# Kernel optimization log

Measured on AMD Instinct MI355X. Metric: run time of the kernel, lower is better.

Reference implementation:

```python
import jax, jax.numpy as jnp
import numpy as np

D_MODEL = 1024
N_HEADS = 16
D_K = D_MODEL // N_HEADS
ROPE_THETA = 10000.0


def setup_inputs() -> dict:
    key = jax.random.key(0)
    ks = jax.random.split(key, 5)
    B, S = 2, 2048
    std = (2.0 / (D_MODEL + D_MODEL)) ** 0.5
    x = jax.random.normal(ks[0], (B, S, D_MODEL), dtype=jnp.float32)
    Wq = jax.random.normal(ks[1], (D_MODEL, D_MODEL), dtype=jnp.float32) * std
    Wk = jax.random.normal(ks[2], (D_MODEL, D_MODEL), dtype=jnp.float32) * std
    Wv = jax.random.normal(ks[3], (D_MODEL, D_MODEL), dtype=jnp.float32) * std
    Wo = jax.random.normal(ks[4], (D_MODEL, D_MODEL), dtype=jnp.float32) * std
    token_positions = jnp.arange(S, dtype=jnp.int64 if jax.config.jax_enable_x64 else jnp.int32)
    return {"x": x, "Wq": Wq, "Wk": Wk, "Wv": Wv, "Wo": Wo,
            "token_positions": token_positions}


def _apply_rope(t, token_positions):
    # t: [B, H, S, d_k]; token_positions: [S]
    inv_freq = 1.0 / (ROPE_THETA ** (jnp.arange(0, D_K, 2, dtype=jnp.float32) / D_K))  # [d_k/2]
    freqs = token_positions.astype(jnp.float32)[:, None] * inv_freq[None, :]  # [S, d_k/2]
    cos, sin = jnp.cos(freqs), jnp.sin(freqs)
    x1, x2 = t[..., ::2], t[..., 1::2]
    xr = x1 * cos - x2 * sin
    yr = x1 * sin + x2 * cos
    # interleave back to even/odd positions
    out = jnp.stack([xr, yr], axis=-1).reshape(t.shape)
    return out


def reference(x, Wq, Wk, Wv, Wo, token_positions):
    B, S, D = x.shape
    H, dk = N_HEADS, D_K
    # projections: weight is [d_out, d_in], applied as x @ W.T
    def proj_heads(W):
        y = jnp.einsum('bsd,ed->bse', x, W)
        return y.reshape(B, S, H, dk).transpose(0, 2, 1, 3)  # [B,H,S,dk]
    q = proj_heads(Wq)
    k = proj_heads(Wk)
    v = proj_heads(Wv)
    q = _apply_rope(q, token_positions)
    k = _apply_rope(k, token_positions)
    scores = jnp.einsum('bhqd,bhkd->bhqk', q, k) / jnp.sqrt(jnp.float32(dk))
    causal = jnp.tril(jnp.ones((S, S), dtype=bool))
    scores = jnp.where(causal, scores, -jnp.inf)
    attn = jax.nn.softmax(scores, axis=-1)
    out = jnp.einsum('bhqk,bhkd->bhqd', attn, v)  # [B,H,S,dk]
    out = out.transpose(0, 2, 1, 3).reshape(B, S, D)
    return jnp.einsum('bsd,ed->bse', out, Wo)
```

## Files before the change

### kernel.cpp

```cpp
#include <hip/hip_runtime.h>

typedef __bf16 bf16x8 __attribute__((ext_vector_type(8)));
typedef float f32x4 __attribute__((ext_vector_type(4)));
typedef unsigned short u16x8 __attribute__((ext_vector_type(8)));


__device__ __forceinline__ unsigned short f2bf(float f) {
  unsigned u = __builtin_bit_cast(unsigned, f);
  u = (u + 0x7FFFu + ((u >> 16) & 1u)) >> 16;
  return (unsigned short)u;
}

__device__ __forceinline__ float bf2f(unsigned short v) {
  return __builtin_bit_cast(float, ((unsigned)v) << 16);
}

__device__ __forceinline__ unsigned cvt_pk_bf16(float lo, float hi) {
  unsigned r;
  asm("v_cvt_pk_bf16_f32 %0, %1, %2" : "=v"(r) : "v"(lo), "v"(hi));
  return r;
}

__device__ __forceinline__ void load_lds16(const void* g, void* l) {
  __builtin_amdgcn_global_load_lds(
      (__attribute__((address_space(1))) void*)g,
      (__attribute__((address_space(3))) void*)l, 16, 0, 0);
}

__global__ __launch_bounds__(256) void k_convert(
    const float* __restrict__ x,
    const float* __restrict__ wq, const float* __restrict__ wk,
    const float* __restrict__ wv, const float* __restrict__ wo,
    unsigned short* __restrict__ xb,
    unsigned short* __restrict__ wqb, unsigned short* __restrict__ wkb,
    unsigned short* __restrict__ wvb, unsigned short* __restrict__ wob) {
  const int g = blockIdx.x * 256 + threadIdx.x;
  const float* src;
  unsigned short* dst;
  int off;
  if (g < (1 << 20)) {
    src = x; dst = xb; off = g;
  } else {
    const int q = g - (1 << 20);
    const int t = q >> 18;
    off = q & ((1 << 18) - 1);
    src = (t == 0) ? wq : (t == 1) ? wk : (t == 2) ? wv : wo;
    dst = (t == 0) ? wqb : (t == 1) ? wkb : (t == 2) ? wvb : wob;
  }
  const float4 v = ((const float4*)src)[off];
  ushort4 r;
  r.x = f2bf(v.x); r.y = f2bf(v.y); r.z = f2bf(v.z); r.w = f2bf(v.w);
  ((ushort4*)dst)[off] = r;
}

__global__ __launch_bounds__(256) void k_rope_tab(const int* __restrict__ tpos,
                                                  float* __restrict__ ct,
                                                  float* __restrict__ st) {
  const int idx = blockIdx.x * 256 + threadIdx.x;
  const int s = idx >> 5, i = idx & 31;
  const double p = (double)tpos[s];
  const double f = p * pow(10000.0, -(double)(2 * i) / 64.0);
  ct[idx] = (float)cos(f);
  st[idx] = (float)sin(f);
}

__device__ __forceinline__ void gemm_core_1024(
    const unsigned short* __restrict__ Ag,
    const unsigned short* __restrict__ Bg,
    unsigned short* As, unsigned short* Bs, f32x4 (&acc)[4][4], int tid) {
  const int lane = tid & 63;
  const int w = tid >> 6;
  const int wm = (w >> 1) * 64;
  const int wn = (w & 1) * 64;
  const int lr = lane & 15;
  const int lg8 = (lane >> 4) * 8;
  const int c0 = tid, c1 = 256 + tid;
  const int ar0 = c0 >> 2, ac0 = (c0 & 3) * 8;
  const int ar1 = c1 >> 2, ac1 = (c1 & 3) * 8;

  auto stage = [&](int buf, int kt) {
    unsigned short* Ab = As + buf * 4096;
    unsigned short* Bb = Bs + buf * 4096;
    load_lds16(Ag + ar0 * 1024 + kt + ac0, Ab + c0 * 8);
    load_lds16(Ag + ar1 * 1024 + kt + ac1, Ab + c1 * 8);
    load_lds16(Bg + ar0 * 1024 + kt + ac0, Bb + c0 * 8);
    load_lds16(Bg + ar1 * 1024 + kt + ac1, Bb + c1 * 8);
  };

  stage(0, 0);
  stage(1, 32);
  int cur = 0;
  for (int ki = 0; ki < 32; ++ki) {
    if (ki + 2 < 32) {
      int nb = cur + 2; if (nb >= 3) nb -= 3;
      stage(nb, (ki + 2) * 32);
      asm volatile("s_waitcnt vmcnt(8)" ::: "memory");
    } else if (ki + 1 < 32) {
      asm volatile("s_waitcnt vmcnt(4)" ::: "memory");
    } else {
      asm volatile("s_waitcnt vmcnt(0)" ::: "memory");
    }
    __builtin_amdgcn_s_barrier();
    const unsigned short* Ab = As + cur * 4096;
    const unsigned short* Bb = Bs + cur * 4096;
    bf16x8 af[4], bfv[4];
#pragma unroll
    for (int mi = 0; mi < 4; ++mi)
      af[mi] = *(const bf16x8*)(Ab + (wm + mi * 16 + lr) * 32 + lg8);
#pragma unroll
    for (int ni = 0; ni < 4; ++ni)
      bfv[ni] = *(const bf16x8*)(Bb + (wn + ni * 16 + lr) * 32 + lg8);
    __builtin_amdgcn_s_setprio(1);
#pragma unroll
    for (int mi = 0; mi < 4; ++mi)
#pragma unroll
      for (int ni = 0; ni < 4; ++ni)
        acc[mi][ni] = __builtin_amdgcn_mfma_f32_16x16x32_bf16(
            af[mi], bfv[ni], acc[mi][ni], 0, 0, 0);
    __builtin_amdgcn_s_setprio(0);
    __builtin_amdgcn_s_barrier();
    ++cur; if (cur == 3) cur = 0;
  }
}

__device__ __forceinline__ void gemm_core_bm64(
    const unsigned short* __restrict__ Ag,
    const unsigned short* __restrict__ Bg,
    unsigned short* As, unsigned short* Bs, f32x4 (&acc)[2][4], int tid) {
  const int lane = tid & 63;
  const int w = tid >> 6;
  const int wm = (w >> 1) * 32;
  const int wn = (w & 1) * 64;
  const int lr = lane & 15;
  const int lg8 = (lane >> 4) * 8;
  const int ar = tid >> 2, ac = (tid & 3) * 8;
  const int c0 = tid, c1 = 256 + tid;
  const int br0 = c0 >> 2, bc0 = (c0 & 3) * 8;
  const int br1 = c1 >> 2, bc1 = (c1 & 3) * 8;

  auto stage = [&](int buf, int kt) {
    load_lds16(Ag + ar * 1024 + kt + ac, As + buf * 2048 + tid * 8);
    load_lds16(Bg + br0 * 1024 + kt + bc0, Bs + buf * 4096 + c0 * 8);
    load_lds16(Bg + br1 * 1024 + kt + bc1, Bs + buf * 4096 + c1 * 8);
  };

  stage(0, 0);
  stage(1, 32);
  int cur = 0;
  for (int ki = 0; ki < 32; ++ki) {
    if (ki + 2 < 32) {
      int nb = cur + 2; if (nb >= 3) nb -= 3;
      stage(nb, (ki + 2) * 32);
      asm volatile("s_waitcnt vmcnt(6)" ::: "memory");
    } else if (ki + 1 < 32) {
      asm volatile("s_waitcnt vmcnt(3)" ::: "memory");
    } else {
      asm volatile("s_waitcnt vmcnt(0)" ::: "memory");
    }
    __builtin_amdgcn_s_barrier();
    const unsigned short* Ab = As + cur * 2048;
    const unsigned short* Bb = Bs + cur * 4096;
    bf16x8 af[2], bfv[4];
#pragma unroll
    for (int mi = 0; mi < 2; ++mi)
      af[mi] = *(const bf16x8*)(Ab + (wm + mi * 16 + lr) * 32 + lg8);
#pragma unroll
    for (int ni = 0; ni < 4; ++ni)
      bfv[ni] = *(const bf16x8*)(Bb + (wn + ni * 16 + lr) * 32 + lg8);
    __builtin_amdgcn_s_setprio(1);
#pragma unroll
    for (int mi = 0; mi < 2; ++mi)
#pragma unroll
      for (int ni = 0; ni < 4; ++ni)
        acc[mi][ni] = __builtin_amdgcn_mfma_f32_16x16x32_bf16(
            af[mi], bfv[ni], acc[mi][ni], 0, 0, 0);
    __builtin_amdgcn_s_setprio(0);
    __builtin_amdgcn_s_barrier();
    ++cur; if (cur == 3) cur = 0;
  }
}

__global__ __launch_bounds__(256) void k_proj(
    const unsigned short* __restrict__ Xb,
    const unsigned short* __restrict__ Wq, const unsigned short* __restrict__ Wk,
    const unsigned short* __restrict__ Wv,
    const float* __restrict__ ctab, const float* __restrict__ stab,
    unsigned short* __restrict__ Qo, unsigned short* __restrict__ Ko,
    unsigned short* __restrict__ Vo) {
  __shared__ __align__(16) unsigned short As[3 * 128 * 32];
  __shared__ __align__(16) unsigned short Bs[3 * 128 * 32];
  const int z = blockIdx.z;
  const unsigned short* Wsel = (z == 0) ? Wq : (z == 1) ? Wk : Wv;
  unsigned short* Out = (z == 0) ? Qo : (z == 1) ? Ko : Vo;
  const int tid = threadIdx.x;
  const int bm = blockIdx.x * 128, bn = blockIdx.y * 128;
  f32x4 acc[4][4] = {};
  gemm_core_1024(Xb + (size_t)bm * 1024, Wsel + (size_t)bn * 1024, As, Bs, acc, tid);

  const int lane = tid & 63, w = tid >> 6;
  const int wm = (w >> 1) * 64, wn = (w & 1) * 64;
  const int lr = lane & 15, lg = lane >> 4;

  if (z == 2) {
#pragma unroll
    for (int mi = 0; mi < 4; ++mi) {
      const int r0 = bm + wm + mi * 16 + lg * 4;
      const int s = r0 & 2047, b = r0 >> 11;
#pragma unroll
      for (int ni = 0; ni < 4; ++ni) {
        const int e = bn + wn + ni * 16 + lr;
        const int h = e >> 6, d = e & 63;
        ushort4 pk;
        pk.x = f2bf(acc[mi][ni][0]);
        pk.y = f2bf(acc[mi][ni][1]);
        pk.z = f2bf(acc[mi][ni][2]);
        pk.w = f2bf(acc[mi][ni][3]);
        *(ushort4*)&Out[((size_t)(b * 16 + h) * 64 + d) * 2048 + s] = pk;
      }
    }
    return;
  }

  const bool odd = lane & 1;
#pragma unroll
  for (int mi = 0; mi < 4; ++mi) {
#pragma unroll
    for (int ni = 0; ni < 4; ++ni) {
#pragma unroll
      for (int reg = 0; reg < 4; ++reg) {
        const int r = bm + wm + mi * 16 + lg * 4 + reg;
        const int e = bn + wn + ni * 16 + lr;
        float val = acc[mi][ni][reg];
        const float partner = __shfl_xor(val, 1);
        const int s = r & 2047, b = r >> 11;
        const int h = e >> 6, d = e & 63;
        const int i = d >> 1;
        const float c = ctab[s * 32 + i];
        const float sn = stab[s * 32 + i];
        const float outv = odd ? (val * c + partner * sn) : (val * c - partner * sn);
        Out[((size_t)(b * 16 + h) * 2048 + s) * 64 + d] = f2bf(outv);
      }
    }
  }
}

__global__ __launch_bounds__(64, 4) void k_attn(
    const unsigned short* __restrict__ Q, const unsigned short* __restrict__ K,
    const unsigned short* __restrict__ Vt, unsigned short* __restrict__ O,
    unsigned short* __restrict__ OpLo, unsigned short* __restrict__ OpHi,
    float2* __restrict__ mlLo, float2* __restrict__ mlHi) {
  __shared__ __align__(16) unsigned short Vs[64 * 64];
  __shared__ __align__(16) unsigned short Pl[16 * 64];
  const int L = blockIdx.x;
  const int i = L >> 3;
  const int bh = (L & 7) * 4 + (i & 3);
  const int c = i >> 2;
  int s, k0, k1, mode;
  if (c < 60) {
    s = 127 - c; const int T = (s * 16 + 79) >> 6; k0 = T >> 1; k1 = T; mode = 2;
  } else if (c < 120) {
    s = 127 - (c - 60); const int T = (s * 16 + 79) >> 6; k0 = 0; k1 = T >> 1; mode = 1;
  } else {
    s = 187 - c; k0 = 0; k1 = (s * 16 + 79) >> 6; mode = 0;
  }
  const int qrow = s * 16;
  const bool masklast = (mode != 1);
  const int lane = threadIdx.x & 63;
  const int lr = lane & 15, lg = lane >> 4;
  const unsigned short* Qg = Q + (size_t)bh * 2048 * 64;
  const unsigned short* Kg = K + (size_t)bh * 2048 * 64;
  const unsigned short* Vg = Vt + (size_t)bh * 64 * 2048;

  bf16x8 qf[2];
#pragma unroll
  for (int h = 0; h < 2; ++h)
    qf[h] = *(const bf16x8*)(Qg + (qrow + lr) * 64 + h * 32 + lg * 8);

  u16x8 ouv;
#pragma unroll
  for (int j = 0; j < 8; ++j) ouv[j] = 0x3F80;
  const bf16x8 onesf = __builtin_bit_cast(bf16x8, ouv);

  f32x4 oacc[4] = {};
  f32x4 la = {};
  float m = -__builtin_inff();

  const float SCL = 0.125f * 1.44269504088896f;

  const int kbase = lr * 64 + lg * 8;
  const int vbase = (lane >> 3) * 2048 + (((lane & 7) ^ (lane >> 3)) * 8);
  const int psw = (lr & 7) << 3;

  auto issueV = [&](int kv) {
    const unsigned short* src = Vg + kv * 64 + vbase;
    unsigned short* dst = &Vs[0] + lane * 8;
#pragma unroll
    for (int i0 = 0; i0 < 8; ++i0)
      load_lds16(src + i0 * 16384, dst + i0 * 512);
  };

  issueV(k0);
  for (int t = k0; t < k1; ++t) {
    bf16x8 kb[4][2];
    {
      const unsigned short* base = Kg + (size_t)t * 4096 + kbase;
#pragma unroll
      for (int nt = 0; nt < 4; ++nt)
#pragma unroll
        for (int h = 0; h < 2; ++h)
          kb[nt][h] = *(const bf16x8*)(base + nt * 1024 + h * 32);
    }

    f32x4 sacc[4];
    __builtin_amdgcn_s_setprio(1);
#pragma unroll
    for (int nt = 0; nt < 4; ++nt) {
      f32x4 z = {0.f, 0.f, 0.f, 0.f};
      z = __builtin_amdgcn_mfma_f32_16x16x32_bf16(kb[nt][0], qf[0], z, 0, 0, 0);
      sacc[nt] = __builtin_amdgcn_mfma_f32_16x16x32_bf16(kb[nt][1], qf[1], z, 0, 0, 0);
    }
    __builtin_amdgcn_s_setprio(0);

    if (masklast && t == k1 - 1) {
      const int qg = qrow + lr;
#pragma unroll
      for (int nt = 0; nt < 4; ++nt)
#pragma unroll
        for (int reg = 0; reg < 4; ++reg) {
          const int kg = t * 64 + nt * 16 + lg * 4 + reg;
          if (kg > qg) sacc[nt][reg] = -__builtin_inff();
        }
    }

    float t0 = fmaxf(fmaxf(sacc[0][0], sacc[0][1]), fmaxf(sacc[0][2], sacc[0][3]));
    float t1 = fmaxf(fmaxf(sacc[1][0], sacc[1][1]), fmaxf(sacc[1][2], sacc[1][3]));
    float t2 = fmaxf(fmaxf(sacc[2][0], sacc[2][1]), fmaxf(sacc[2][2], sacc[2][3]));
    float t3 = fmaxf(fmaxf(sacc[3][0], sacc[3][1]), fmaxf(sacc[3][2], sacc[3][3]));
    float pm = fmaxf(fmaxf(t0, t1), fmaxf(t2, t3));
    pm = fmaxf(pm, __shfl_xor(pm, 16));
    pm = fmaxf(pm, __shfl_xor(pm, 32));
    if (__any(pm > m)) {
      const float mn = fmaxf(m, pm);
      const float al = exp2f(SCL * (m - mn));
      m = mn;
#pragma unroll
      for (int reg = 0; reg < 4; ++reg) la[reg] *= al;
#pragma unroll
      for (int nt = 0; nt < 4; ++nt)
#pragma unroll
        for (int reg = 0; reg < 4; ++reg) oacc[nt][reg] *= al;
    }
    const float msc = SCL * m;

#pragma unroll
    for (int nt = 0; nt < 4; ++nt) {
      const float p0 = exp2f(sacc[nt][0] * SCL - msc);
      const float p1 = exp2f(sacc[nt][1] * SCL - msc);
      const float p2 = exp2f(sacc[nt][2] * SCL - msc);
      const float p3 = exp2f(sacc[nt][3] * SCL - msc);
      const unsigned w01 = cvt_pk_bf16(p0, p1);
      const unsigned w23 = cvt_pk_bf16(p2, p3);
      ushort4 pk;
      pk.x = (unsigned short)w01; pk.y = (unsigned short)(w01 >> 16);
      pk.z = (unsigned short)w23; pk.w = (unsigned short)(w23 >> 16);
      *(ushort4*)(Pl + lr * 64 + ((nt * 16 + lg * 4) ^ psw)) = pk;
    }
    bf16x8 pa[2];
#pragma unroll
    for (int ks = 0; ks < 2; ++ks)
      pa[ks] = *(const bf16x8*)(Pl + lr * 64 + ((ks * 32 + lg * 8) ^ psw));

    asm volatile("s_waitcnt vmcnt(0)" ::: "memory");

    __builtin_amdgcn_s_setprio(1);
    la = __builtin_amdgcn_mfma_f32_16x16x32_bf16(onesf, pa[0], la, 0, 0, 0);
    la = __builtin_amdgcn_mfma_f32_16x16x32_bf16(onesf, pa[1], la, 0, 0, 0);
#pragma unroll
    for (int nt = 0; nt < 4; ++nt) {
      const int row = nt * 16 + lr;
      const bf16x8 vb0 = *(const bf16x8*)(Vs + row * 64 + ((lg ^ (row & 7)) * 8));
      const bf16x8 vb1 = *(const bf16x8*)(Vs + row * 64 + (((lg + 4) ^ (row & 7)) * 8));
      oacc[nt] = __builtin_amdgcn_mfma_f32_16x16x32_bf16(vb0, pa[0], oacc[nt], 0, 0, 0);
      oacc[nt] = __builtin_amdgcn_mfma_f32_16x16x32_bf16(vb1, pa[1], oacc[nt], 0, 0, 0);
    }
    __builtin_amdgcn_s_setprio(0);

    asm volatile("s_waitcnt lgkmcnt(0)" ::: "memory");
    if (t + 1 < k1) issueV(t + 1);
  }

  const int b = bh >> 4, h = bh & 15;
  if (mode == 0) {
    const float inv = 1.0f / la[0];
    unsigned short* dst = &O[((size_t)b * 2048 + qrow + lr) * 1024 + h * 64];
#pragma unroll
    for (int nt = 0; nt < 4; ++nt) {
      const unsigned w01 = cvt_pk_bf16(oacc[nt][0] * inv, oacc[nt][1] * inv);
      const unsigned w23 = cvt_pk_bf16(oacc[nt][2] * inv, oacc[nt][3] * inv);
      ushort4 pk;
      pk.x = (unsigned short)w01; pk.y = (unsigned short)(w01 >> 16);
      pk.z = (unsigned short)w23; pk.w = (unsigned short)(w23 >> 16);
      *(ushort4*)(dst + nt * 16 + lg * 4) = pk;
    }
  } else {
    const int idx = bh * 60 + (s - 68);
    unsigned short* dst = (mode == 1 ? OpLo : OpHi) + idx * 1024 + lr * 64;
#pragma unroll
    for (int nt = 0; nt < 4; ++nt) {
      const unsigned w01 = cvt_pk_bf16(oacc[nt][0], oacc[nt][1]);
      const unsigned w23 = cvt_pk_bf16(oacc[nt][2], oacc[nt][3]);
      ushort4 pk;
      pk.x = (unsigned short)w01; pk.y = (unsigned short)(w01 >> 16);
      pk.z = (unsigned short)w23; pk.w = (unsigned short)(w23 >> 16);
      *(ushort4*)(dst + nt * 16 + lg * 4) = pk;
    }
    if (lane < 16)
      (mode == 1 ? mlLo : mlHi)[idx * 16 + lr] = make_float2(m, la[0]);
  }
}

__global__ __launch_bounds__(256) void k_merge(
    const unsigned short* __restrict__ OpLo, const unsigned short* __restrict__ OpHi,
    const float2* __restrict__ mlLo, const float2* __restrict__ mlHi,
    unsigned short* __restrict__ O) {
  const int g = blockIdx.x * 4 + (threadIdx.x >> 6);
  const int lane = threadIdx.x & 63;
  const int bh = g / 60, sr = g - bh * 60;
  const int s = 68 + sr;
  const int q = lane & 15, dblk = lane >> 4;
  const float SCL = 0.125f * 1.44269504088896f;
  const float2 a = mlLo[g * 16 + q];
  const float2 bm = mlHi[g * 16 + q];
  const float mm = fmaxf(a.x, bm.x);
  const float wl = exp2f(SCL * (a.x - mm));
  const float wh = exp2f(SCL * (bm.x - mm));
  const float inv = 1.0f / (a.y * wl + bm.y * wh);
  const int off = g * 1024 + q * 64 + dblk * 16;
  const u16x8 lo0 = *(const u16x8*)(OpLo + off);
  const u16x8 lo1 = *(const u16x8*)(OpLo + off + 8);
  const u16x8 hi0 = *(const u16x8*)(OpHi + off);
  const u16x8 hi1 = *(const u16x8*)(OpHi + off + 8);
  const int b = bh >> 4, h = bh & 15;
  unsigned short* dst = &O[((size_t)b * 2048 + s * 16 + q) * 1024 + h * 64 + dblk * 16];
  u16x8 r0, r1;
#pragma unroll
  for (int j = 0; j < 8; j += 2) {
    const float f0 = (bf2f(lo0[j]) * wl + bf2f(hi0[j]) * wh) * inv;
    const float f1 = (bf2f(lo0[j + 1]) * wl + bf2f(hi0[j + 1]) * wh) * inv;
    const unsigned wpk = cvt_pk_bf16(f0, f1);
    r0[j] = (unsigned short)wpk; r0[j + 1] = (unsigned short)(wpk >> 16);
    const float g0 = (bf2f(lo1[j]) * wl + bf2f(hi1[j]) * wh) * inv;
    const float g1 = (bf2f(lo1[j + 1]) * wl + bf2f(hi1[j + 1]) * wh) * inv;
    const unsigned wpk2 = cvt_pk_bf16(g0, g1);
    r1[j] = (unsigned short)wpk2; r1[j + 1] = (unsigned short)(wpk2 >> 16);
  }
  *(u16x8*)dst = r0;
  *(u16x8*)(dst + 8) = r1;
}

__global__ __launch_bounds__(256) void k_out(const unsigned short* __restrict__ Ab,
                                             const unsigned short* __restrict__ Wo,
                                             float* __restrict__ Out) {
  __shared__ __align__(16) unsigned short As[3 * 64 * 32];
  __shared__ __align__(16) unsigned short Bs[3 * 128 * 32];
  const int tid = threadIdx.x;
  const int bm = blockIdx.x * 64, bn = blockIdx.y * 128;
  f32x4 acc[2][4] = {};
  gemm_core_bm64(Ab + (size_t)bm * 1024, Wo + (size_t)bn * 1024, As, Bs, acc, tid);
  const int lane = tid & 63, w = tid >> 6;
  const int wm = (w >> 1) * 32, wn = (w & 1) * 64;
  const int lr = lane & 15, lg = lane >> 4;
#pragma unroll
  for (int mi = 0; mi < 2; ++mi)
#pragma unroll
    for (int ni = 0; ni < 4; ++ni)
#pragma unroll
      for (int reg = 0; reg < 4; ++reg) {
        const int r = bm + wm + mi * 16 + lg * 4 + reg;
        const int e = bn + wn + ni * 16 + lr;
        Out[(size_t)r * 1024 + e] = acc[mi][ni][reg];
      }
}

extern "C" void kernel_launch(void* const* d_in, const int* in_sizes, int n_in,
                              void* d_out, int out_size, void* d_ws, size_t ws_size,
                              hipStream_t stream) {
  const float* x = (const float*)d_in[0];
  const float* Wq = (const float*)d_in[1];
  const float* Wk = (const float*)d_in[2];
  const float* Wv = (const float*)d_in[3];
  const float* Wo = (const float*)d_in[4];
  const int* tpos = (const int*)d_in[5];
  float* out = (float*)d_out;
  char* ws = (char*)d_ws;
  const size_t MB = 1024 * 1024;
  unsigned short* xb = (unsigned short*)(ws);
  unsigned short* wqb = (unsigned short*)(ws + 8 * MB);
  unsigned short* wkb = (unsigned short*)(ws + 10 * MB);
  unsigned short* wvb = (unsigned short*)(ws + 12 * MB);
  unsigned short* wob = (unsigned short*)(ws + 14 * MB);
  unsigned short* Qb = (unsigned short*)(ws + 16 * MB);
  unsigned short* Kb = (unsigned short*)(ws + 24 * MB);
  unsigned short* Vtb = (unsigned short*)(ws + 32 * MB);
  unsigned short* Ab = (unsigned short*)(ws + 40 * MB);
  float* ctab = (float*)(ws + 48 * MB);
  float* stab = (float*)(ws + 48 * MB + 256 * 1024);
  unsigned short* OpLo = (unsigned short*)(ws);
  unsigned short* OpHi = (unsigned short*)(ws + 4 * MB);
  float2* mlLo = (float2*)(ws + 8 * MB);
  float2* mlHi = (float2*)(ws + 9 * MB);

  k_convert<<<dim3(8192), dim3(256), 0, stream>>>(x, Wq, Wk, Wv, Wo, xb, wqb, wkb,
                                                  wvb, wob);
  k_rope_tab<<<dim3(256), dim3(256), 0, stream>>>(tpos, ctab, stab);
  k_proj<<<dim3(32, 8, 3), dim3(256), 0, stream>>>(xb, wqb, wkb, wvb, ctab, stab,
                                                   Qb, Kb, Vtb);
  k_attn<<<dim3(6016), dim3(64), 0, stream>>>(Qb, Kb, Vtb, Ab, OpLo, OpHi, mlLo,
                                              mlHi);
  k_merge<<<dim3(480), dim3(256), 0, stream>>>(OpLo, OpHi, mlLo, mlHi, Ab);
  k_out<<<dim3(64, 8), dim3(256), 0, stream>>>(Ab, wob, out);
}
```

Baseline: 174.0 us.

## Drop split-KV attention and merge kernel; load V directly into registers

Removes the split-KV scheme in which long query tiles were split into two partial passes and combined by a separate merge kernel. Each 16-row query tile is now handled by one wave over its whole causal KV range, with a simple block index mapping and 4096 blocks. V tiles are loaded straight from global memory into registers instead of asynchronously staged through LDS, and the P scratch buffer uses row padding in place of XOR swizzling. This saves a kernel launch and the partial-result traffic, but reintroduces load imbalance between short and long tiles and loses the V prefetch overlap.

After: 210.3 us. 20.9% more time.

```diff
diff --git a/kernel.cpp b/kernel.cpp
--- a/kernel.cpp
+++ b/kernel.cpp
@@ -9,10 +9,6 @@
   unsigned u = __builtin_bit_cast(unsigned, f);
   u = (u + 0x7FFFu + ((u >> 16) & 1u)) >> 16;
   return (unsigned short)u;
-}
-
-__device__ __forceinline__ float bf2f(unsigned short v) {
-  return __builtin_bit_cast(float, ((unsigned)v) << 16);
 }
 
 __device__ __forceinline__ unsigned cvt_pk_bf16(float lo, float hi) {
@@ -246,25 +242,13 @@
 
 __global__ __launch_bounds__(64, 4) void k_attn(
     const unsigned short* __restrict__ Q, const unsigned short* __restrict__ K,
-    const unsigned short* __restrict__ Vt, unsigned short* __restrict__ O,
-    unsigned short* __restrict__ OpLo, unsigned short* __restrict__ OpHi,
-    float2* __restrict__ mlLo, float2* __restrict__ mlHi) {
-  __shared__ __align__(16) unsigned short Vs[64 * 64];
-  __shared__ __align__(16) unsigned short Pl[16 * 64];
+    const unsigned short* __restrict__ Vt, unsigned short* __restrict__ O) {
+  __shared__ __align__(16) unsigned short Pl[16 * 68];
   const int L = blockIdx.x;
-  const int i = L >> 3;
-  const int bh = (L & 7) * 4 + (i & 3);
-  const int c = i >> 2;
-  int s, k0, k1, mode;
-  if (c < 60) {
-    s = 127 - c; const int T = (s * 16 + 79) >> 6; k0 = T >> 1; k1 = T; mode = 2;
-  } else if (c < 120) {
-    s = 127 - (c - 60); const int T = (s * 16 + 79) >> 6; k0 = 0; k1 = T >> 1; mode = 1;
-  } else {
-    s = 187 - c; k0 = 0; k1 = (s * 16 + 79) >> 6; mode = 0;
-  }
+  const int bh = (L & 7) * 4 + ((L >> 3) & 3);
+  const int s = L >> 5;
   const int qrow = s * 16;
-  const bool masklast = (mode != 1);
+  const int T = (qrow + 79) >> 6;
   const int lane = threadIdx.x & 63;
   const int lr = lane & 15, lg = lane >> 4;
   const unsigned short* Qg = Q + (size_t)bh * 2048 * 64;
@@ -288,27 +272,26 @@
   const float SCL = 0.125f * 1.44269504088896f;
 
   const int kbase = lr * 64 + lg * 8;
-  const int vbase = (lane >> 3) * 2048 + (((lane & 7) ^ (lane >> 3)) * 8);
-  const int psw = (lr & 7) << 3;
-
-  auto issueV = [&](int kv) {
-    const unsigned short* src = Vg + kv * 64 + vbase;
-    unsigned short* dst = &Vs[0] + lane * 8;
-#pragma unroll
-    for (int i0 = 0; i0 < 8; ++i0)
-      load_lds16(src + i0 * 16384, dst + i0 * 512);
-  };
-
-  issueV(k0);
-  for (int t = k0; t < k1; ++t) {
-    bf16x8 kb[4][2];
+  const int vbase = lr * 2048 + lg * 8;
+
+  for (int t = 0; t < T; ++t) {
+    bf16x8 vf[4][2];
+    {
+      const unsigned short* base = Vg + vbase + t * 64;
+#pragma unroll
+      for (int nt = 0; nt < 4; ++nt)
+#pragma unroll
+        for (int ks = 0; ks < 2; ++ks)
+          vf[nt][ks] = *(const bf16x8*)(base + nt * 16 * 2048 + ks * 32);
+    }
+    bf16x8 kf[4][2];
     {
       const unsigned short* base = Kg + (size_t)t * 4096 + kbase;
 #pragma unroll
       for (int nt = 0; nt < 4; ++nt)
 #pragma unroll
         for (int h = 0; h < 2; ++h)
-          kb[nt][h] = *(const bf16x8*)(base + nt * 1024 + h * 32);
+          kf[nt][h] = *(const bf16x8*)(base + nt * 1024 + h * 32);
     }
 
     f32x4 sacc[4];
@@ -316,12 +299,12 @@
 #pragma unroll
     for (int nt = 0; nt < 4; ++nt) {
       f32x4 z = {0.f, 0.f, 0.f, 0.f};
-      z = __builtin_amdgcn_mfma_f32_16x16x32_bf16(kb[nt][0], qf[0], z, 0, 0, 0);
-      sacc[nt] = __builtin_amdgcn_mfma_f32_16x16x32_bf16(kb[nt][1], qf[1], z, 0, 0, 0);
+      z = __builtin_amdgcn_mfma_f32_16x16x32_bf16(kf[nt][0], qf[0], z, 0, 0, 0);
+      sacc[nt] = __builtin_amdgcn_mfma_f32_16x16x32_bf16(kf[nt][1], qf[1], z, 0, 0, 0);
     }
     __builtin_amdgcn_s_setprio(0);
 
-    if (masklast && t == k1 - 1) {
+    if (t == T - 1) {
       const int qg = qrow + lr;
 #pragma unroll
       for (int nt = 0; nt < 4; ++nt)
@@ -352,6 +335,7 @@
     }
     const float msc = SCL * m;
 
+    unsigned short* prow = Pl + lr * 68;
 #pragma unroll
     for (int nt = 0; nt < 4; ++nt) {
       const float p0 = exp2f(sacc[nt][0] * SCL - msc);
@@ -363,99 +347,36 @@
       ushort4 pk;
       pk.x = (unsigned short)w01; pk.y = (unsigned short)(w01 >> 16);
       pk.z = (unsigned short)w23; pk.w = (unsigned short)(w23 >> 16);
-      *(ushort4*)(Pl + lr * 64 + ((nt * 16 + lg * 4) ^ psw)) = pk;
+      *(ushort4*)(prow + nt * 16 + lg * 4) = pk;
     }
     bf16x8 pa[2];
 #pragma unroll
     for (int ks = 0; ks < 2; ++ks)
-      pa[ks] = *(const bf16x8*)(Pl + lr * 64 + ((ks * 32 + lg * 8) ^ psw));
-
-    asm volatile("s_waitcnt vmcnt(0)" ::: "memory");
+      pa[ks] = *(const bf16x8*)(Pl + lr * 68 + ks * 32 + lg * 8);
 
     __builtin_amdgcn_s_setprio(1);
     la = __builtin_amdgcn_mfma_f32_16x16x32_bf16(onesf, pa[0], la, 0, 0, 0);
     la = __builtin_amdgcn_mfma_f32_16x16x32_bf16(onesf, pa[1], la, 0, 0, 0);
 #pragma unroll
     for (int nt = 0; nt < 4; ++nt) {
-      const int row = nt * 16 + lr;
-      const bf16x8 vb0 = *(const bf16x8*)(Vs + row * 64 + ((lg ^ (row & 7)) * 8));
-      const bf16x8 vb1 = *(const bf16x8*)(Vs + row * 64 + (((lg + 4) ^ (row & 7)) * 8));
-      oacc[nt] = __builtin_amdgcn_mfma_f32_16x16x32_bf16(vb0, pa[0], oacc[nt], 0, 0, 0);
-      oacc[nt] = __builtin_amdgcn_mfma_f32_16x16x32_bf16(vb1, pa[1], oacc[nt], 0, 0, 0);
+      oacc[nt] = __builtin_amdgcn_mfma_f32_16x16x32_bf16(vf[nt][0], pa[0], oacc[nt], 0, 0, 0);
+      oacc[nt] = __builtin_amdgcn_mfma_f32_16x16x32_bf16(vf[nt][1], pa[1], oacc[nt], 0, 0, 0);
     }
     __builtin_amdgcn_s_setprio(0);
-
-    asm volatile("s_waitcnt lgkmcnt(0)" ::: "memory");
-    if (t + 1 < k1) issueV(t + 1);
   }
 
   const int b = bh >> 4, h = bh & 15;
-  if (mode == 0) {
-    const float inv = 1.0f / la[0];
-    unsigned short* dst = &O[((size_t)b * 2048 + qrow + lr) * 1024 + h * 64];
-#pragma unroll
-    for (int nt = 0; nt < 4; ++nt) {
-      const unsigned w01 = cvt_pk_bf16(oacc[nt][0] * inv, oacc[nt][1] * inv);
-      const unsigned w23 = cvt_pk_bf16(oacc[nt][2] * inv, oacc[nt][3] * inv);
-      ushort4 pk;
-      pk.x = (unsigned short)w01; pk.y = (unsigned short)(w01 >> 16);
-      pk.z = (unsigned short)w23; pk.w = (unsigned short)(w23 >> 16);
-      *(ushort4*)(dst + nt * 16 + lg * 4) = pk;
-    }
-  } else {
-    const int idx = bh * 60 + (s - 68);
-    unsigned short* dst = (mode == 1 ? OpLo : OpHi) + idx * 1024 + lr * 64;
-#pragma unroll
-    for (int nt = 0; nt < 4; ++nt) {
-      const unsigned w01 = cvt_pk_bf16(oacc[nt][0], oacc[nt][1]);
-      const unsigned w23 = cvt_pk_bf16(oacc[nt][2], oacc[nt][3]);
-      ushort4 pk;
-      pk.x = (unsigned short)w01; pk.y = (unsigned short)(w01 >> 16);
-      pk.z = (unsigned short)w23; pk.w = (unsigned short)(w23 >> 16);
-      *(ushort4*)(dst + nt * 16 + lg * 4) = pk;
-    }
-    if (lane < 16)
-      (mode == 1 ? mlLo : mlHi)[idx * 16 + lr] = make_float2(m, la[0]);
-  }
-}
-
-__global__ __launch_bounds__(256) void k_merge(
-    const unsigned short* __restrict__ OpLo, const unsigned short* __restrict__ OpHi,
-    const float2* __restrict__ mlLo, const float2* __restrict__ mlHi,
-    unsigned short* __restrict__ O) {
-  const int g = blockIdx.x * 4 + (threadIdx.x >> 6);
-  const int lane = threadIdx.x & 63;
-  const int bh = g / 60, sr = g - bh * 60;
-  const int s = 68 + sr;
-  const int q = lane & 15, dblk = lane >> 4;
-  const float SCL = 0.125f * 1.44269504088896f;
-  const float2 a = mlLo[g * 16 + q];
-  const float2 bm = mlHi[g * 16 + q];
-  const float mm = fmaxf(a.x, bm.x);
-  const float wl = exp2f(SCL * (a.x - mm));
-  const float wh = exp2f(SCL * (bm.x - mm));
-  const float inv = 1.0f / (a.y * wl + bm.y * wh);
-  const int off = g * 1024 + q * 64 + dblk * 16;
-  const u16x8 lo0 = *(const u16x8*)(OpLo + off);
-  const u16x8 lo1 = *(const u16x8*)(OpLo + off + 8);
-  const u16x8 hi0 = *(const u16x8*)(OpHi + off);
-  const u16x8 hi1 = *(const u16x8*)(OpHi + off + 8);
-  const int b = bh >> 4, h = bh & 15;
-  unsigned short* dst = &O[((size_t)b * 2048 + s * 16 + q) * 1024 + h * 64 + dblk * 16];
-  u16x8 r0, r1;
-#pragma unroll
-  for (int j = 0; j < 8; j += 2) {
-    const float f0 = (bf2f(lo0[j]) * wl + bf2f(hi0[j]) * wh) * inv;
-    const float f1 = (bf2f(lo0[j + 1]) * wl + bf2f(hi0[j + 1]) * wh) * inv;
-    const unsigned wpk = cvt_pk_bf16(f0, f1);
-    r0[j] = (unsigned short)wpk; r0[j + 1] = (unsigned short)(wpk >> 16);
-    const float g0 = (bf2f(lo1[j]) * wl + bf2f(hi1[j]) * wh) * inv;
-    const float g1 = (bf2f(lo1[j + 1]) * wl + bf2f(hi1[j + 1]) * wh) * inv;
-    const unsigned wpk2 = cvt_pk_bf16(g0, g1);
-    r1[j] = (unsigned short)wpk2; r1[j + 1] = (unsigned short)(wpk2 >> 16);
-  }
-  *(u16x8*)dst = r0;
-  *(u16x8*)(dst + 8) = r1;
+  const float inv = 1.0f / la[0];
+  unsigned short* dst = &O[((size_t)b * 2048 + qrow + lr) * 1024 + h * 64];
+#pragma unroll
+  for (int nt = 0; nt < 4; ++nt) {
+    const unsigned w01 = cvt_pk_bf16(oacc[nt][0] * inv, oacc[nt][1] * inv);
+    const unsigned w23 = cvt_pk_bf16(oacc[nt][2] * inv, oacc[nt][3] * inv);
+    ushort4 pk;
+    pk.x = (unsigned short)w01; pk.y = (unsigned short)(w01 >> 16);
+    pk.z = (unsigned short)w23; pk.w = (unsigned short)(w23 >> 16);
+    *(ushort4*)(dst + nt * 16 + lg * 4) = pk;
+  }
 }
 
 __global__ __launch_bounds__(256) void k_out(const unsigned short* __restrict__ Ab,
@@ -505,18 +426,12 @@
   unsigned short* Ab = (unsigned short*)(ws + 40 * MB);
   float* ctab = (float*)(ws + 48 * MB);
   float* stab = (float*)(ws + 48 * MB + 256 * 1024);
-  unsigned short* OpLo = (unsigned short*)(ws);
-  unsigned short* OpHi = (unsigned short*)(ws + 4 * MB);
-  float2* mlLo = (float2*)(ws + 8 * MB);
-  float2* mlHi = (float2*)(ws + 9 * MB);
 
   k_convert<<<dim3(8192), dim3(256), 0, stream>>>(x, Wq, Wk, Wv, Wo, xb, wqb, wkb,
                                                   wvb, wob);
   k_rope_tab<<<dim3(256), dim3(256), 0, stream>>>(tpos, ctab, stab);
   k_proj<<<dim3(32, 8, 3), dim3(256), 0, stream>>>(xb, wqb, wkb, wvb, ctab, stab,
                                                    Qb, Kb, Vtb);
-  k_attn<<<dim3(6016), dim3(64), 0, stream>>>(Qb, Kb, Vtb, Ab, OpLo, OpHi, mlLo,
-                                              mlHi);
-  k_merge<<<dim3(480), dim3(256), 0, stream>>>(OpLo, OpHi, mlLo, mlHi, Ab);
+  k_attn<<<dim3(4096), dim3(64), 0, stream>>>(Qb, Kb, Vtb, Ab);
   k_out<<<dim3(64, 8), dim3(256), 0, stream>>>(Ab, wob, out);
 }
```
